# Performance work log

Measured on AMD Instinct MI355X. Metric: run time of the kernel, lower is better.

The kernel has to match this reference:

```python
import jax, jax.numpy as jnp
import numpy as np

# Multi-level feature-map spatial shapes (compile-time constants, as in Deformable DETR
# for an 800x1333 input with strides 8/16/32/64).
SPATIAL_SHAPES = ((100, 167), (50, 84), (25, 42), (13, 21))
NUM_KEYS = sum(h * w for h, w in SPATIAL_SHAPES)  # 22223


def setup_inputs() -> dict:
    key = jax.random.key(0)
    k1, k2, k3 = jax.random.split(key, 3)
    bs, nq, nh, d, nl, npt = 8, 900, 8, 32, 4, 4
    value = jax.random.normal(k1, (bs, NUM_KEYS, nh, d), jnp.float32)
    sampling_locations = jax.random.uniform(k2, (bs, nq, nh, nl, npt, 2), jnp.float32)
    aw = jax.random.uniform(k3, (bs, nq, nh, nl, npt), jnp.float32)
    # module applies softmax over (levels*points) before calling the kernel
    aw = jax.nn.softmax(aw.reshape(bs, nq, nh, nl * npt), axis=-1).reshape(bs, nq, nh, nl, npt)
    return {"value": value, "sampling_locations": sampling_locations, "attention_weights": aw}


def _bilinear_sample(v_flat, H, W, x, y):
    # v_flat: (bs, nh, H*W, d); x, y: (bs, nh, P) pixel coords (align_corners=False convention)
    x0 = jnp.floor(x)
    y0 = jnp.floor(y)
    x1 = x0 + 1.0
    y1 = y0 + 1.0
    wx1 = x - x0
    wx0 = 1.0 - wx1
    wy1 = y - y0
    wy0 = 1.0 - wy1

    def gather(xi, yi):
        # zero padding: out-of-bounds corners contribute 0 (grid_sample padding_mode='zeros')
        valid = (xi >= 0) & (xi <= W - 1) & (yi >= 0) & (yi <= H - 1)
        xc = jnp.clip(xi, 0, W - 1).astype(jnp.int32)
        yc = jnp.clip(yi, 0, H - 1).astype(jnp.int32)
        idx = yc * W + xc  # (bs, nh, P)
        s = jnp.take_along_axis(v_flat, idx[..., None], axis=2)  # (bs, nh, P, d)
        return jnp.where(valid[..., None], s, jnp.zeros((), v_flat.dtype))

    return (gather(x0, y0) * (wx0 * wy0)[..., None]
            + gather(x1, y0) * (wx1 * wy0)[..., None]
            + gather(x0, y1) * (wx0 * wy1)[..., None]
            + gather(x1, y1) * (wx1 * wy1)[..., None])


def reference(value, sampling_locations, attention_weights):
    # value: (bs, num_keys, nh, d)
    # sampling_locations: (bs, nq, nh, nl, npt, 2), normalized (x, y) in [0, 1]
    # attention_weights: (bs, nq, nh, nl, npt)
    bs, _, nh, d = value.shape
    _, nq, _, nl, npt, _ = sampling_locations.shape
    out = jnp.zeros((bs, nh, nq, d), value.dtype)
    start = 0
    for lvl, (H, W) in enumerate(SPATIAL_SHAPES):
        v = value[:, start:start + H * W]                     # (bs, H*W, nh, d)
        start += H * W
        v = jnp.transpose(v, (0, 2, 1, 3))                    # (bs, nh, H*W, d)
        loc = sampling_locations[:, :, :, lvl]                # (bs, nq, nh, npt, 2)
        # grid = 2*loc - 1; pixel coord (align_corners=False): (g+1)*S/2 - 0.5 = loc*S - 0.5
        x = loc[..., 0] * W - 0.5
        y = loc[..., 1] * H - 0.5
        x = jnp.transpose(x, (0, 2, 1, 3)).reshape(bs, nh, nq * npt)
        y = jnp.transpose(y, (0, 2, 1, 3)).reshape(bs, nh, nq * npt)
        sampled = _bilinear_sample(v, H, W, x, y).reshape(bs, nh, nq, npt, d)
        w = jnp.transpose(attention_weights[:, :, :, lvl], (0, 2, 1, 3))  # (bs, nh, nq, npt)
        out = out + jnp.einsum('bhqpd,bhqp->bhqd', sampled, w)
    # torch output is (bs, nq, nh*d) with head-major channel layout
    return jnp.transpose(out, (0, 2, 1, 3)).reshape(bs, nq, nh * d)
```

## Files before the change

kernel.cpp:

```cpp
#include <hip/hip_runtime.h>


#define BS 8
#define NQ 900
#define NH 8
#define NL 4
#define NPT 4
#define NUM_KEYS 22223
#define QCHUNKS 113

__global__ __launch_bounds__(256) void msda_kernel(
    const float* __restrict__ value,
    const float* __restrict__ loc,
    const float* __restrict__ aw,
    float* __restrict__ out)
{
    const int x  = blockIdx.x & 7;
    const int t  = blockIdx.x >> 3;
    const int b  = t / QCHUNKS;
    const int qc = t - b * QCHUNKS;
    const int h  = x;

    const int cg  = threadIdx.x & 7;
    const int lvl = (threadIdx.x >> 3) & 3;
    const int qs  = threadIdx.x >> 5;
    const int q   = qc * 8 + qs;
    if (q >= NQ) return;

    const bool l01 = lvl < 2;
    const int H  = l01 ? (lvl == 0 ? 100 : 50)  : (lvl == 2 ? 25 : 13);
    const int W  = l01 ? (lvl == 0 ? 167 : 84)  : (lvl == 2 ? 42 : 21);
    const int St = l01 ? (lvl == 0 ? 0 : 16700) : (lvl == 2 ? 20900 : 21950);

    const float4* __restrict__ v4 = (const float4*)value;
    const unsigned vbase = (unsigned)b * (NUM_KEYS * NH * 8) + h * 8 + cg
                         + (unsigned)St * (NH * 8);
    const unsigned rowstride = (unsigned)W * (NH * 8);

    const int lidx = ((b * NQ + q) * NH + h) * NL + lvl;
    const float4* __restrict__ loc4 = (const float4*)loc;
    const float4* __restrict__ aw4  = (const float4*)aw;
    const float4 xy01 = loc4[lidx * 2];
    const float4 xy23 = loc4[lidx * 2 + 1];
    const float4 wv   = aw4[lidx];

    const float xs[NPT] = {xy01.x, xy01.z, xy23.x, xy23.z};
    const float ys[NPT] = {xy01.y, xy01.w, xy23.y, xy23.w};
    const float ws[NPT] = {wv.x, wv.y, wv.z, wv.w};

    float4 acc = {0.f, 0.f, 0.f, 0.f};

    #pragma unroll
    for (int p = 0; p < NPT; ++p) {
        const float xf = xs[p] * (float)W - 0.5f;
        const float yf = ys[p] * (float)H - 0.5f;
        const float w  = ws[p];
        const float fx0 = floorf(xf);
        const float fy0 = floorf(yf);
        const int x0 = (int)fx0;
        const int y0 = (int)fy0;
        float wx1 = xf - fx0, wy1 = yf - fy0;
        float wx0 = 1.f - wx1, wy0 = 1.f - wy1;

        wx0 = (x0 >= 0 && x0 <= W - 1)         ? wx0 : 0.f;
        wx1 = (x0 + 1 >= 0 && x0 + 1 <= W - 1) ? wx1 : 0.f;
        wy0 = (y0 >= 0 && y0 <= H - 1)         ? wy0 : 0.f;
        wy1 = (y0 + 1 >= 0 && y0 + 1 <= H - 1) ? wy1 : 0.f;

        const int x0c = min(max(x0, 0), W - 1);
        const int x1c = min(max(x0 + 1, 0), W - 1);
        const int y0c = min(max(y0, 0), H - 1);
        const int y1c = min(max(y0 + 1, 0), H - 1);

        const unsigned r0 = vbase + (unsigned)y0c * rowstride;
        const unsigned r1 = vbase + (unsigned)y1c * rowstride;

        const float4 v00 = v4[r0 + (unsigned)x0c * (NH * 8)];
        const float4 v01 = v4[r0 + (unsigned)x1c * (NH * 8)];
        const float4 v10 = v4[r1 + (unsigned)x0c * (NH * 8)];
        const float4 v11 = v4[r1 + (unsigned)x1c * (NH * 8)];

        const float s00 = w * wx0 * wy0;
        const float s01 = w * wx1 * wy0;
        const float s10 = w * wx0 * wy1;
        const float s11 = w * wx1 * wy1;

        acc.x = fmaf(s00, v00.x, acc.x); acc.y = fmaf(s00, v00.y, acc.y);
        acc.z = fmaf(s00, v00.z, acc.z); acc.w = fmaf(s00, v00.w, acc.w);
        acc.x = fmaf(s01, v01.x, acc.x); acc.y = fmaf(s01, v01.y, acc.y);
        acc.z = fmaf(s01, v01.z, acc.z); acc.w = fmaf(s01, v01.w, acc.w);
        acc.x = fmaf(s10, v10.x, acc.x); acc.y = fmaf(s10, v10.y, acc.y);
        acc.z = fmaf(s10, v10.z, acc.z); acc.w = fmaf(s10, v10.w, acc.w);
        acc.x = fmaf(s11, v11.x, acc.x); acc.y = fmaf(s11, v11.y, acc.y);
        acc.z = fmaf(s11, v11.z, acc.z); acc.w = fmaf(s11, v11.w, acc.w);
    }

    acc.x += __shfl_xor(acc.x, 8);  acc.y += __shfl_xor(acc.y, 8);
    acc.z += __shfl_xor(acc.z, 8);  acc.w += __shfl_xor(acc.w, 8);
    acc.x += __shfl_xor(acc.x, 16); acc.y += __shfl_xor(acc.y, 16);
    acc.z += __shfl_xor(acc.z, 16); acc.w += __shfl_xor(acc.w, 16);

    if (lvl == 0) {
        float4* __restrict__ out4 = (float4*)out;
        out4[((b * NQ + q) * NH + h) * 8 + cg] = acc;
    }
}

extern "C" void kernel_launch(void* const* d_in, const int* in_sizes, int n_in,
                              void* d_out, int out_size, void* d_ws, size_t ws_size,
                              hipStream_t stream) {
    const float* value = (const float*)d_in[0];
    const float* loc   = (const float*)d_in[1];
    const float* aw    = (const float*)d_in[2];
    float* outp = (float*)d_out;

    const int grid = 8 * BS * QCHUNKS;
    msda_kernel<<<grid, 256, 0, stream>>>(value, loc, aw, outp);
}
```

Measured before the change: 271.5 us.

## Split sampling into separate level-0 and coarse-level kernels to improve cache locality

Replaces the single kernel, which mapped one level per 8-thread group and reduced across levels with shuffles, with two launches. The first samples only the large level 0 and writes the output. The second loops over the three small levels per thread and adds into the output written by the first. The intent is that each pass works on a smaller, more cache-resident part of the value tensor, and that the cross-lane shuffle reduction goes away. In exchange it adds a second launch and an extra read-modify-write of the output.

```diff
diff --git a/kernel.cpp b/kernel.cpp
--- a/kernel.cpp
+++ b/kernel.cpp
@@ -7,103 +7,142 @@
 #define NL 4
 #define NPT 4
 #define NUM_KEYS 22223
-#define QCHUNKS 113
+#define QC_B 29
 
-__global__ __launch_bounds__(256) void msda_kernel(
+__device__ __forceinline__ float4 bilin_acc(
+    const float4* __restrict__ v4, float4 acc,
+    unsigned vbase, unsigned rowstride, int H, int W,
+    float xn, float yn, float w)
+{
+    const float xf = xn * (float)W - 0.5f;
+    const float yf = yn * (float)H - 0.5f;
+    const float fx0 = floorf(xf);
+    const float fy0 = floorf(yf);
+    const int x0 = (int)fx0;
+    const int y0 = (int)fy0;
+    float wx1 = xf - fx0, wy1 = yf - fy0;
+    float wx0 = 1.f - wx1, wy0 = 1.f - wy1;
+
+    wx0 = (x0 >= 0 && x0 <= W - 1)         ? wx0 : 0.f;
+    wx1 = (x0 + 1 >= 0 && x0 + 1 <= W - 1) ? wx1 : 0.f;
+    wy0 = (y0 >= 0 && y0 <= H - 1)         ? wy0 : 0.f;
+    wy1 = (y0 + 1 >= 0 && y0 + 1 <= H - 1) ? wy1 : 0.f;
+
+    const int x0c = min(max(x0, 0), W - 1);
+    const int x1c = min(max(x0 + 1, 0), W - 1);
+    const int y0c = min(max(y0, 0), H - 1);
+    const int y1c = min(max(y0 + 1, 0), H - 1);
+
+    const unsigned r0 = vbase + (unsigned)y0c * rowstride;
+    const unsigned r1 = vbase + (unsigned)y1c * rowstride;
+
+    const float4 v00 = v4[r0 + (unsigned)x0c * (NH * 8)];
+    const float4 v01 = v4[r0 + (unsigned)x1c * (NH * 8)];
+    const float4 v10 = v4[r1 + (unsigned)x0c * (NH * 8)];
+    const float4 v11 = v4[r1 + (unsigned)x1c * (NH * 8)];
+
+    const float s00 = w * wx0 * wy0;
+    const float s01 = w * wx1 * wy0;
+    const float s10 = w * wx0 * wy1;
+    const float s11 = w * wx1 * wy1;
+
+    acc.x = fmaf(s00, v00.x, acc.x); acc.y = fmaf(s00, v00.y, acc.y);
+    acc.z = fmaf(s00, v00.z, acc.z); acc.w = fmaf(s00, v00.w, acc.w);
+    acc.x = fmaf(s01, v01.x, acc.x); acc.y = fmaf(s01, v01.y, acc.y);
+    acc.z = fmaf(s01, v01.z, acc.z); acc.w = fmaf(s01, v01.w, acc.w);
+    acc.x = fmaf(s10, v10.x, acc.x); acc.y = fmaf(s10, v10.y, acc.y);
+    acc.z = fmaf(s10, v10.z, acc.z); acc.w = fmaf(s10, v10.w, acc.w);
+    acc.x = fmaf(s11, v11.x, acc.x); acc.y = fmaf(s11, v11.y, acc.y);
+    acc.z = fmaf(s11, v11.z, acc.z); acc.w = fmaf(s11, v11.w, acc.w);
+    return acc;
+}
+
+__global__ __launch_bounds__(256) void msda_lvl0(
+    const float* __restrict__ value,
+    const float* __restrict__ loc,
+    const float* __restrict__ aw,
+    float* __restrict__ out)
+{
+    const int tid = blockIdx.x * 256 + threadIdx.x;
+    const int cg = tid & 7;
+    const int h  = (tid >> 3) & 7;
+    const int bq = tid >> 6;
+    const int b  = bq / NQ;
+
+    const int H = 100, W = 167;
+    const float4* __restrict__ v4 = (const float4*)value;
+    const unsigned vbase = (unsigned)b * (NUM_KEYS * NH * 8) + h * 8 + cg;
+    const unsigned rowstride = (unsigned)W * (NH * 8);
+
+    const int lidx = (bq * NH + h) * NL + 0;
+    const float4* __restrict__ loc4 = (const float4*)loc;
+    const float4* __restrict__ aw4  = (const float4*)aw;
+    const float4 xy01 = loc4[lidx * 2];
+    const float4 xy23 = loc4[lidx * 2 + 1];
+    const float4 wv   = aw4[lidx];
+
+    float4 acc = {0.f, 0.f, 0.f, 0.f};
+    acc = bilin_acc(v4, acc, vbase, rowstride, H, W, xy01.x, xy01.y, wv.x);
+    acc = bilin_acc(v4, acc, vbase, rowstride, H, W, xy01.z, xy01.w, wv.y);
+    acc = bilin_acc(v4, acc, vbase, rowstride, H, W, xy23.x, xy23.y, wv.z);
+    acc = bilin_acc(v4, acc, vbase, rowstride, H, W, xy23.z, xy23.w, wv.w);
+
+    float4* __restrict__ out4 = (float4*)out;
+    out4[(bq * NH + h) * 8 + cg] = acc;
+}
+
+__global__ __launch_bounds__(256) void msda_lvl123(
     const float* __restrict__ value,
     const float* __restrict__ loc,
     const float* __restrict__ aw,
     float* __restrict__ out)
 {
     const int x  = blockIdx.x & 7;
-    const int t  = blockIdx.x >> 3;
-    const int b  = t / QCHUNKS;
-    const int qc = t - b * QCHUNKS;
+    const int j  = blockIdx.x >> 3;
+    const int b  = j / QC_B;
+    const int qc = j - b * QC_B;
     const int h  = x;
 
-    const int cg  = threadIdx.x & 7;
-    const int lvl = (threadIdx.x >> 3) & 3;
-    const int qs  = threadIdx.x >> 5;
-    const int q   = qc * 8 + qs;
+    const int cg = threadIdx.x & 7;
+    const int qs = threadIdx.x >> 3;
+    const int q  = qc * 32 + qs;
     if (q >= NQ) return;
 
-    const bool l01 = lvl < 2;
-    const int H  = l01 ? (lvl == 0 ? 100 : 50)  : (lvl == 2 ? 25 : 13);
-    const int W  = l01 ? (lvl == 0 ? 167 : 84)  : (lvl == 2 ? 42 : 21);
-    const int St = l01 ? (lvl == 0 ? 0 : 16700) : (lvl == 2 ? 20900 : 21950);
+    const float4* __restrict__ v4 = (const float4*)value;
+    const unsigned vb0 = (unsigned)b * (NUM_KEYS * NH * 8) + h * 8 + cg;
 
-    const float4* __restrict__ v4 = (const float4*)value;
-    const unsigned vbase = (unsigned)b * (NUM_KEYS * NH * 8) + h * 8 + cg
-                         + (unsigned)St * (NH * 8);
-    const unsigned rowstride = (unsigned)W * (NH * 8);
-
-    const int lidx = ((b * NQ + q) * NH + h) * NL + lvl;
     const float4* __restrict__ loc4 = (const float4*)loc;
     const float4* __restrict__ aw4  = (const float4*)aw;
-    const float4 xy01 = loc4[lidx * 2];
-    const float4 xy23 = loc4[lidx * 2 + 1];
-    const float4 wv   = aw4[lidx];
-
-    const float xs[NPT] = {xy01.x, xy01.z, xy23.x, xy23.z};
-    const float ys[NPT] = {xy01.y, xy01.w, xy23.y, xy23.w};
-    const float ws[NPT] = {wv.x, wv.y, wv.z, wv.w};
+    const int lbase = ((b * NQ + q) * NH + h) * NL;
 
     float4 acc = {0.f, 0.f, 0.f, 0.f};
 
+    const int Hs[3]  = {50, 25, 13};
+    const int Ws[3]  = {84, 42, 21};
+    const int Sts[3] = {16700, 20900, 21950};
+
     #pragma unroll
-    for (int p = 0; p < NPT; ++p) {
-        const float xf = xs[p] * (float)W - 0.5f;
-        const float yf = ys[p] * (float)H - 0.5f;
-        const float w  = ws[p];
-        const float fx0 = floorf(xf);
-        const float fy0 = floorf(yf);
-        const int x0 = (int)fx0;
-        const int y0 = (int)fy0;
-        float wx1 = xf - fx0, wy1 = yf - fy0;
-        float wx0 = 1.f - wx1, wy0 = 1.f - wy1;
+    for (int li = 0; li < 3; ++li) {
+        const int H = Hs[li], W = Ws[li];
+        const unsigned vbase = vb0 + (unsigned)Sts[li] * (NH * 8);
+        const unsigned rowstride = (unsigned)W * (NH * 8);
 
-        wx0 = (x0 >= 0 && x0 <= W - 1)         ? wx0 : 0.f;
-        wx1 = (x0 + 1 >= 0 && x0 + 1 <= W - 1) ? wx1 : 0.f;
-        wy0 = (y0 >= 0 && y0 <= H - 1)         ? wy0 : 0.f;
-        wy1 = (y0 + 1 >= 0 && y0 + 1 <= H - 1) ? wy1 : 0.f;
+        const int lidx = lbase + (li + 1);
+        const float4 xy01 = loc4[lidx * 2];
+        const float4 xy23 = loc4[lidx * 2 + 1];
+        const float4 wv   = aw4[lidx];
 
-        const int x0c = min(max(x0, 0), W - 1);
-        const int x1c = min(max(x0 + 1, 0), W - 1);
-        const int y0c = min(max(y0, 0), H - 1);
-        const int y1c = min(max(y0 + 1, 0), H - 1);
-
-        const unsigned r0 = vbase + (unsigned)y0c * rowstride;
-        const unsigned r1 = vbase + (unsigned)y1c * rowstride;
-
-        const float4 v00 = v4[r0 + (unsigned)x0c * (NH * 8)];
-        const float4 v01 = v4[r0 + (unsigned)x1c * (NH * 8)];
-        const float4 v10 = v4[r1 + (unsigned)x0c * (NH * 8)];
-        const float4 v11 = v4[r1 + (unsigned)x1c * (NH * 8)];
-
-        const float s00 = w * wx0 * wy0;
-        const float s01 = w * wx1 * wy0;
-        const float s10 = w * wx0 * wy1;
-        const float s11 = w * wx1 * wy1;
-
-        acc.x = fmaf(s00, v00.x, acc.x); acc.y = fmaf(s00, v00.y, acc.y);
-        acc.z = fmaf(s00, v00.z, acc.z); acc.w = fmaf(s00, v00.w, acc.w);
-        acc.x = fmaf(s01, v01.x, acc.x); acc.y = fmaf(s01, v01.y, acc.y);
-        acc.z = fmaf(s01, v01.z, acc.z); acc.w = fmaf(s01, v01.w, acc.w);
-        acc.x = fmaf(s10, v10.x, acc.x); acc.y = fmaf(s10, v10.y, acc.y);
-        acc.z = fmaf(s10, v10.z, acc.z); acc.w = fmaf(s10, v10.w, acc.w);
-        acc.x = fmaf(s11, v11.x, acc.x); acc.y = fmaf(s11, v11.y, acc.y);
-        acc.z = fmaf(s11, v11.z, acc.z); acc.w = fmaf(s11, v11.w, acc.w);
+        acc = bilin_acc(v4, acc, vbase, rowstride, H, W, xy01.x, xy01.y, wv.x);
+        acc = bilin_acc(v4, acc, vbase, rowstride, H, W, xy01.z, xy01.w, wv.y);
+        acc = bilin_acc(v4, acc, vbase, rowstride, H, W, xy23.x, xy23.y, wv.z);
+        acc = bilin_acc(v4, acc, vbase, rowstride, H, W, xy23.z, xy23.w, wv.w);
     }
 
-    acc.x += __shfl_xor(acc.x, 8);  acc.y += __shfl_xor(acc.y, 8);
-    acc.z += __shfl_xor(acc.z, 8);  acc.w += __shfl_xor(acc.w, 8);
-    acc.x += __shfl_xor(acc.x, 16); acc.y += __shfl_xor(acc.y, 16);
-    acc.z += __shfl_xor(acc.z, 16); acc.w += __shfl_xor(acc.w, 16);
-
-    if (lvl == 0) {
-        float4* __restrict__ out4 = (float4*)out;
-        out4[((b * NQ + q) * NH + h) * 8 + cg] = acc;
-    }
+    float4* __restrict__ out4 = (float4*)out;
+    const int oidx = ((b * NQ + q) * NH + h) * 8 + cg;
+    const float4 prev = out4[oidx];
+    acc.x += prev.x; acc.y += prev.y; acc.z += prev.z; acc.w += prev.w;
+    out4[oidx] = acc;
 }
 
 extern "C" void kernel_launch(void* const* d_in, const int* in_sizes, int n_in,
@@ -114,6 +153,6 @@
     const float* aw    = (const float*)d_in[2];
     float* outp = (float*)d_out;
 
-    const int grid = 8 * BS * QCHUNKS;
-    msda_kernel<<<grid, 256, 0, stream>>>(value, loc, aw, outp);
+    msda_lvl0<<<1800, 256, 0, stream>>>(value, loc, aw, outp);
+    msda_lvl123<<<8 * BS * QC_B, 256, 0, stream>>>(value, loc, aw, outp);
 }
```

After: 281.5 us. 3.7% more time.

## Stage coarse levels in LDS as fp16 and give each thread all levels

Applied to the files above, without the earlier changes.

Each block now covers one (batch, head) pair and 113 queries with 1024 threads. At startup it copies the two coarsest levels' value slice (1323 keys) into shared memory as fp16, and those two levels are then sampled from LDS while levels 0 and 1 still read from global memory. Each thread now handles all four levels for one query and channel group, so the shuffle reduction goes away. The intent is to cut repeated global gathers for the small levels, at the cost of fp16 rounding error, a per-block preload, and only 512 blocks running at one block per CU.

```diff
diff --git a/kernel.cpp b/kernel.cpp
--- a/kernel.cpp
+++ b/kernel.cpp
@@ -1,109 +1,201 @@
 #include <hip/hip_runtime.h>
+#include <hip/hip_fp16.h>
 
 
 #define BS 8
 #define NQ 900
 #define NH 8
 #define NL 4
-#define NPT 4
 #define NUM_KEYS 22223
-#define QCHUNKS 113
-
-__global__ __launch_bounds__(256) void msda_kernel(
+#define QPB 113
+#define ST23 20900
+#define NLINES 1323
+#define LDS_BYTES (NLINES * 32 * 2)
+
+__device__ __forceinline__ float4 bilin_g(
+    const float4* __restrict__ v4, float4 acc,
+    unsigned vbase, unsigned rowstride, int H, int W,
+    float xn, float yn, float w)
+{
+    const float xf = xn * (float)W - 0.5f;
+    const float yf = yn * (float)H - 0.5f;
+    const float fx0 = floorf(xf);
+    const float fy0 = floorf(yf);
+    const int x0 = (int)fx0;
+    const int y0 = (int)fy0;
+    float wx1 = xf - fx0, wy1 = yf - fy0;
+    float wx0 = 1.f - wx1, wy0 = 1.f - wy1;
+
+    wx0 = (x0 >= 0 && x0 <= W - 1)         ? wx0 : 0.f;
+    wx1 = (x0 + 1 >= 0 && x0 + 1 <= W - 1) ? wx1 : 0.f;
+    wy0 = (y0 >= 0 && y0 <= H - 1)         ? wy0 : 0.f;
+    wy1 = (y0 + 1 >= 0 && y0 + 1 <= H - 1) ? wy1 : 0.f;
+
+    const int x0c = min(max(x0, 0), W - 1);
+    const int x1c = min(max(x0 + 1, 0), W - 1);
+    const int y0c = min(max(y0, 0), H - 1);
+    const int y1c = min(max(y0 + 1, 0), H - 1);
+
+    const unsigned r0 = vbase + (unsigned)y0c * rowstride;
+    const unsigned r1 = vbase + (unsigned)y1c * rowstride;
+
+    const float4 v00 = v4[r0 + (unsigned)x0c * (NH * 8)];
+    const float4 v01 = v4[r0 + (unsigned)x1c * (NH * 8)];
+    const float4 v10 = v4[r1 + (unsigned)x0c * (NH * 8)];
+    const float4 v11 = v4[r1 + (unsigned)x1c * (NH * 8)];
+
+    const float s00 = w * wx0 * wy0;
+    const float s01 = w * wx1 * wy0;
+    const float s10 = w * wx0 * wy1;
+    const float s11 = w * wx1 * wy1;
+
+    acc.x = fmaf(s00, v00.x, acc.x); acc.y = fmaf(s00, v00.y, acc.y);
+    acc.z = fmaf(s00, v00.z, acc.z); acc.w = fmaf(s00, v00.w, acc.w);
+    acc.x = fmaf(s01, v01.x, acc.x); acc.y = fmaf(s01, v01.y, acc.y);
+    acc.z = fmaf(s01, v01.z, acc.z); acc.w = fmaf(s01, v01.w, acc.w);
+    acc.x = fmaf(s10, v10.x, acc.x); acc.y = fmaf(s10, v10.y, acc.y);
+    acc.z = fmaf(s10, v10.z, acc.z); acc.w = fmaf(s10, v10.w, acc.w);
+    acc.x = fmaf(s11, v11.x, acc.x); acc.y = fmaf(s11, v11.y, acc.y);
+    acc.z = fmaf(s11, v11.z, acc.z); acc.w = fmaf(s11, v11.w, acc.w);
+    return acc;
+}
+
+__device__ __forceinline__ float4 bilin_l(
+    const __half* __restrict__ lv, float4 acc,
+    int lbase, int H, int W, int cg,
+    float xn, float yn, float w)
+{
+    const float xf = xn * (float)W - 0.5f;
+    const float yf = yn * (float)H - 0.5f;
+    const float fx0 = floorf(xf);
+    const float fy0 = floorf(yf);
+    const int x0 = (int)fx0;
+    const int y0 = (int)fy0;
+    float wx1 = xf - fx0, wy1 = yf - fy0;
+    float wx0 = 1.f - wx1, wy0 = 1.f - wy1;
+
+    wx0 = (x0 >= 0 && x0 <= W - 1)         ? wx0 : 0.f;
+    wx1 = (x0 + 1 >= 0 && x0 + 1 <= W - 1) ? wx1 : 0.f;
+    wy0 = (y0 >= 0 && y0 <= H - 1)         ? wy0 : 0.f;
+    wy1 = (y0 + 1 >= 0 && y0 + 1 <= H - 1) ? wy1 : 0.f;
+
+    const int x0c = min(max(x0, 0), W - 1);
+    const int x1c = min(max(x0 + 1, 0), W - 1);
+    const int y0c = min(max(y0, 0), H - 1);
+    const int y1c = min(max(y0 + 1, 0), H - 1);
+
+    const int r0 = lbase + y0c * W;
+    const int r1 = lbase + y1c * W;
+
+    const __half2* p00 = (const __half2*)(lv + (r0 + x0c) * 32 + cg * 4);
+    const __half2* p01 = (const __half2*)(lv + (r0 + x1c) * 32 + cg * 4);
+    const __half2* p10 = (const __half2*)(lv + (r1 + x0c) * 32 + cg * 4);
+    const __half2* p11 = (const __half2*)(lv + (r1 + x1c) * 32 + cg * 4);
+
+    const float2 a00 = __half22float2(p00[0]), b00 = __half22float2(p00[1]);
+    const float2 a01 = __half22float2(p01[0]), b01 = __half22float2(p01[1]);
+    const float2 a10 = __half22float2(p10[0]), b10 = __half22float2(p10[1]);
+    const float2 a11 = __half22float2(p11[0]), b11 = __half22float2(p11[1]);
+
+    const float s00 = w * wx0 * wy0;
+    const float s01 = w * wx1 * wy0;
+    const float s10 = w * wx0 * wy1;
+    const float s11 = w * wx1 * wy1;
+
+    acc.x = fmaf(s00, a00.x, acc.x); acc.y = fmaf(s00, a00.y, acc.y);
+    acc.z = fmaf(s00, b00.x, acc.z); acc.w = fmaf(s00, b00.y, acc.w);
+    acc.x = fmaf(s01, a01.x, acc.x); acc.y = fmaf(s01, a01.y, acc.y);
+    acc.z = fmaf(s01, b01.x, acc.z); acc.w = fmaf(s01, b01.y, acc.w);
+    acc.x = fmaf(s10, a10.x, acc.x); acc.y = fmaf(s10, a10.y, acc.y);
+    acc.z = fmaf(s10, b10.x, acc.z); acc.w = fmaf(s10, b10.y, acc.w);
+    acc.x = fmaf(s11, a11.x, acc.x); acc.y = fmaf(s11, a11.y, acc.y);
+    acc.z = fmaf(s11, b11.x, acc.z); acc.w = fmaf(s11, b11.y, acc.w);
+    return acc;
+}
+
+__global__ __launch_bounds__(1024, 1) void msda_kernel(
     const float* __restrict__ value,
     const float* __restrict__ loc,
     const float* __restrict__ aw,
     float* __restrict__ out)
 {
-    const int x  = blockIdx.x & 7;
-    const int t  = blockIdx.x >> 3;
-    const int b  = t / QCHUNKS;
-    const int qc = t - b * QCHUNKS;
-    const int h  = x;
-
-    const int cg  = threadIdx.x & 7;
-    const int lvl = (threadIdx.x >> 3) & 3;
-    const int qs  = threadIdx.x >> 5;
-    const int q   = qc * 8 + qs;
-    if (q >= NQ) return;
-
-    const bool l01 = lvl < 2;
-    const int H  = l01 ? (lvl == 0 ? 100 : 50)  : (lvl == 2 ? 25 : 13);
-    const int W  = l01 ? (lvl == 0 ? 167 : 84)  : (lvl == 2 ? 42 : 21);
-    const int St = l01 ? (lvl == 0 ? 0 : 16700) : (lvl == 2 ? 20900 : 21950);
+    extern __shared__ __half lv[];
+
+    const int bh = blockIdx.x & 63;
+    const int qb = blockIdx.x >> 6;
+    const int b  = bh >> 3;
+    const int h  = bh & 7;
 
     const float4* __restrict__ v4 = (const float4*)value;
-    const unsigned vbase = (unsigned)b * (NUM_KEYS * NH * 8) + h * 8 + cg
-                         + (unsigned)St * (NH * 8);
-    const unsigned rowstride = (unsigned)W * (NH * 8);
-
-    const int lidx = ((b * NQ + q) * NH + h) * NL + lvl;
+
+    const unsigned sbase = (unsigned)(b * NUM_KEYS + ST23) * (NH * 8) + h * 8;
+    for (int i = threadIdx.x; i < NLINES * 8; i += 1024) {
+        const int key = i >> 3;
+        const int sub = i & 7;
+        const float4 v = v4[sbase + (unsigned)key * (NH * 8) + sub];
+        __half2* dst = (__half2*)(lv + i * 4);
+        dst[0] = __floats2half2_rn(v.x, v.y);
+        dst[1] = __floats2half2_rn(v.z, v.w);
+    }
+    __syncthreads();
+
+    const int cg = threadIdx.x & 7;
+    const int tq = threadIdx.x >> 3;
+    const int q0 = qb * QPB;
+    const int qcount = min(NQ - q0, QPB);
+    if (tq >= qcount) return;
+    const int q = q0 + tq;
+
+    const unsigned vb0 = (unsigned)b * (NUM_KEYS * NH * 8) + h * 8 + cg;
+
     const float4* __restrict__ loc4 = (const float4*)loc;
     const float4* __restrict__ aw4  = (const float4*)aw;
-    const float4 xy01 = loc4[lidx * 2];
-    const float4 xy23 = loc4[lidx * 2 + 1];
-    const float4 wv   = aw4[lidx];
-
-    const float xs[NPT] = {xy01.x, xy01.z, xy23.x, xy23.z};
-    const float ys[NPT] = {xy01.y, xy01.w, xy23.y, xy23.w};
-    const float ws[NPT] = {wv.x, wv.y, wv.z, wv.w};
+    const int lbase = ((b * NQ + q) * NH + h) * NL;
 
     float4 acc = {0.f, 0.f, 0.f, 0.f};
 
-    #pragma unroll
-    for (int p = 0; p < NPT; ++p) {
-        const float xf = xs[p] * (float)W - 0.5f;
-        const float yf = ys[p] * (float)H - 0.5f;
-        const float w  = ws[p];
-        const float fx0 = floorf(xf);
-        const float fy0 = floorf(yf);
-        const int x0 = (int)fx0;
-        const int y0 = (int)fy0;
-        float wx1 = xf - fx0, wy1 = yf - fy0;
-        float wx0 = 1.f - wx1, wy0 = 1.f - wy1;
-
-        wx0 = (x0 >= 0 && x0 <= W - 1)         ? wx0 : 0.f;
-        wx1 = (x0 + 1 >= 0 && x0 + 1 <= W - 1) ? wx1 : 0.f;
-        wy0 = (y0 >= 0 && y0 <= H - 1)         ? wy0 : 0.f;
-        wy1 = (y0 + 1 >= 0 && y0 + 1 <= H - 1) ? wy1 : 0.f;
-
-        const int x0c = min(max(x0, 0), W - 1);
-        const int x1c = min(max(x0 + 1, 0), W - 1);
-        const int y0c = min(max(y0, 0), H - 1);
-        const int y1c = min(max(y0 + 1, 0), H - 1);
-
-        const unsigned r0 = vbase + (unsigned)y0c * rowstride;
-        const unsigned r1 = vbase + (unsigned)y1c * rowstride;
-
-        const float4 v00 = v4[r0 + (unsigned)x0c * (NH * 8)];
-        const float4 v01 = v4[r0 + (unsigned)x1c * (NH * 8)];
-        const float4 v10 = v4[r1 + (unsigned)x0c * (NH * 8)];
-        const float4 v11 = v4[r1 + (unsigned)x1c * (NH * 8)];
-
-        const float s00 = w * wx0 * wy0;
-        const float s01 = w * wx1 * wy0;
-        const float s10 = w * wx0 * wy1;
-        const float s11 = w * wx1 * wy1;
-
-        acc.x = fmaf(s00, v00.x, acc.x); acc.y = fmaf(s00, v00.y, acc.y);
-        acc.z = fmaf(s00, v00.z, acc.z); acc.w = fmaf(s00, v00.w, acc.w);
-        acc.x = fmaf(s01, v01.x, acc.x); acc.y = fmaf(s01, v01.y, acc.y);
-        acc.z = fmaf(s01, v01.z, acc.z); acc.w = fmaf(s01, v01.w, acc.w);
-        acc.x = fmaf(s10, v10.x, acc.x); acc.y = fmaf(s10, v10.y, acc.y);
-        acc.z = fmaf(s10, v10.z, acc.z); acc.w = fmaf(s10, v10.w, acc.w);
-        acc.x = fmaf(s11, v11.x, acc.x); acc.y = fmaf(s11, v11.y, acc.y);
-        acc.z = fmaf(s11, v11.z, acc.z); acc.w = fmaf(s11, v11.w, acc.w);
-    }
-
-    acc.x += __shfl_xor(acc.x, 8);  acc.y += __shfl_xor(acc.y, 8);
-    acc.z += __shfl_xor(acc.z, 8);  acc.w += __shfl_xor(acc.w, 8);
-    acc.x += __shfl_xor(acc.x, 16); acc.y += __shfl_xor(acc.y, 16);
-    acc.z += __shfl_xor(acc.z, 16); acc.w += __shfl_xor(acc.w, 16);
-
-    if (lvl == 0) {
-        float4* __restrict__ out4 = (float4*)out;
-        out4[((b * NQ + q) * NH + h) * 8 + cg] = acc;
-    }
+    {
+        const float4 xy01 = loc4[(lbase + 0) * 2];
+        const float4 xy23 = loc4[(lbase + 0) * 2 + 1];
+        const float4 wv   = aw4[lbase + 0];
+        const unsigned rs = 167u * (NH * 8);
+        acc = bilin_g(v4, acc, vb0, rs, 100, 167, xy01.x, xy01.y, wv.x);
+        acc = bilin_g(v4, acc, vb0, rs, 100, 167, xy01.z, xy01.w, wv.y);
+        acc = bilin_g(v4, acc, vb0, rs, 100, 167, xy23.x, xy23.y, wv.z);
+        acc = bilin_g(v4, acc, vb0, rs, 100, 167, xy23.z, xy23.w, wv.w);
+    }
+    {
+        const float4 xy01 = loc4[(lbase + 1) * 2];
+        const float4 xy23 = loc4[(lbase + 1) * 2 + 1];
+        const float4 wv   = aw4[lbase + 1];
+        const unsigned vb1 = vb0 + 16700u * (NH * 8);
+        const unsigned rs = 84u * (NH * 8);
+        acc = bilin_g(v4, acc, vb1, rs, 50, 84, xy01.x, xy01.y, wv.x);
+        acc = bilin_g(v4, acc, vb1, rs, 50, 84, xy01.z, xy01.w, wv.y);
+        acc = bilin_g(v4, acc, vb1, rs, 50, 84, xy23.x, xy23.y, wv.z);
+        acc = bilin_g(v4, acc, vb1, rs, 50, 84, xy23.z, xy23.w, wv.w);
+    }
+    {
+        const float4 xy01 = loc4[(lbase + 2) * 2];
+        const float4 xy23 = loc4[(lbase + 2) * 2 + 1];
+        const float4 wv   = aw4[lbase + 2];
+        acc = bilin_l(lv, acc, 0, 25, 42, cg, xy01.x, xy01.y, wv.x);
+        acc = bilin_l(lv, acc, 0, 25, 42, cg, xy01.z, xy01.w, wv.y);
+        acc = bilin_l(lv, acc, 0, 25, 42, cg, xy23.x, xy23.y, wv.z);
+        acc = bilin_l(lv, acc, 0, 25, 42, cg, xy23.z, xy23.w, wv.w);
+    }
+    {
+        const float4 xy01 = loc4[(lbase + 3) * 2];
+        const float4 xy23 = loc4[(lbase + 3) * 2 + 1];
+        const float4 wv   = aw4[lbase + 3];
+        acc = bilin_l(lv, acc, 1050, 13, 21, cg, xy01.x, xy01.y, wv.x);
+        acc = bilin_l(lv, acc, 1050, 13, 21, cg, xy01.z, xy01.w, wv.y);
+        acc = bilin_l(lv, acc, 1050, 13, 21, cg, xy23.x, xy23.y, wv.z);
+        acc = bilin_l(lv, acc, 1050, 13, 21, cg, xy23.z, xy23.w, wv.w);
+    }
+
+    float4* __restrict__ out4 = (float4*)out;
+    out4[((b * NQ + q) * NH + h) * 8 + cg] = acc;
 }
 
 extern "C" void kernel_launch(void* const* d_in, const int* in_sizes, int n_in,
@@ -114,6 +206,5 @@
     const float* aw    = (const float*)d_in[2];
     float* outp = (float*)d_out;
 
-    const int grid = 8 * BS * QCHUNKS;
-    msda_kernel<<<grid, 256, 0, stream>>>(value, loc, aw, outp);
-}
+    msda_kernel<<<512, 1024, LDS_BYTES, stream>>>(value, loc, aw, outp);
+}
```

Measured after the change: 272.3 us. About the same (+0.3%).
